# Kernel tuning notes

Measured on AMD Instinct MI355X. Metric: run time of the kernel, lower is better.

Reference implementation:

```python
import jax, jax.numpy as jnp
import numpy as np

EMBED_DIM = 1024
NUM_HEADS = 16
HEAD_DIM = EMBED_DIM // NUM_HEADS


def setup_inputs() -> dict:
    key = jax.random.key(0)
    ks = jax.random.split(key, 11)
    B, S, E = 4, 2048, EMBED_DIM
    s = 1.0 / np.sqrt(E)
    return {
        "q": jax.random.normal(ks[0], (B, S, E), jnp.float32),
        "k": jax.random.normal(ks[1], (B, S, E), jnp.float32),
        "v": jax.random.normal(ks[2], (B, S, E), jnp.float32),
        "Wq": jax.random.uniform(ks[3], (E, E), jnp.float32, -s, s),
        "bq": jax.random.uniform(ks[4], (E,), jnp.float32, -s, s),
        "Wk": jax.random.uniform(ks[5], (E, E), jnp.float32, -s, s),
        "bk": jax.random.uniform(ks[6], (E,), jnp.float32, -s, s),
        "Wv": jax.random.uniform(ks[7], (E, E), jnp.float32, -s, s),
        "bv": jax.random.uniform(ks[8], (E,), jnp.float32, -s, s),
        "Wo": jax.random.uniform(ks[9], (E, E), jnp.float32, -s, s),
        "bo": jax.random.uniform(ks[10], (E,), jnp.float32, -s, s),
    }


def _split_heads(x):
    B, S, E = x.shape
    return x.reshape(B, S, NUM_HEADS, HEAD_DIM).transpose(0, 2, 1, 3)  # [B,H,S,D]


def reference(q, k, v, Wq, bq, Wk, bk, Wv, bv, Wo, bo):
    # torch Linear: x @ W.T + b
    Q = _split_heads(q @ Wq.T + bq)
    K = _split_heads(k @ Wk.T + bk)
    V = _split_heads(v @ Wv.T + bv)
    scale = 1.0 / jnp.sqrt(jnp.float32(HEAD_DIM))
    scores = jnp.einsum("bhqd,bhkd->bhqk", Q, K) * scale  # [B,H,S,S]
    weights = jax.nn.softmax(scores, axis=-1)
    ctx = jnp.einsum("bhqk,bhkd->bhqd", weights, V)
    B, H, S, D = ctx.shape
    merged = ctx.transpose(0, 2, 1, 3).reshape(B, S, H * D)
    out = merged @ Wo.T + bo
    return out, weights
```

## Files before the change

kernel.cpp:

```cpp
#include <hip/hip_runtime.h>
#include <hip/hip_bf16.h>

typedef __bf16 bf16x8 __attribute__((ext_vector_type(8)));
typedef __bf16 bf16x4 __attribute__((ext_vector_type(4)));
typedef float f32x4 __attribute__((ext_vector_type(4)));

constexpr size_t XQ_OFF = 0;
constexpr size_t WQ_OFF = 25165824;
constexpr size_t Q_OFF  = 29360128;
constexpr size_t KK_OFF = 37748736;
constexpr size_t VT_OFF = 46137344;
constexpr size_t CTX_OFF= 54525952;

__device__ __forceinline__ void gload16(const void* g, void* s) {
    __builtin_amdgcn_global_load_lds((__attribute__((address_space(1))) void*)g,
                                     (__attribute__((address_space(3))) void*)s, 16, 0, 0);
}
#define WAIT_VM0()   asm volatile("s_waitcnt vmcnt(0)" ::: "memory")
#define WAIT_VM4()   asm volatile("s_waitcnt vmcnt(4)" ::: "memory")
#define WAIT_VM8()   asm volatile("s_waitcnt vmcnt(8)" ::: "memory")
#define WAIT_LGKM0() asm volatile("s_waitcnt lgkmcnt(0)" ::: "memory")
#define BAR()        __builtin_amdgcn_s_barrier()

__global__ __launch_bounds__(256) void convert_k(
    const float* __restrict__ q, const float* __restrict__ k, const float* __restrict__ v,
    const float* __restrict__ Wq, const float* __restrict__ Wk, const float* __restrict__ Wv,
    const float* __restrict__ Wo, __bf16* __restrict__ ws) {
    int id = blockIdx.x * 256 + threadIdx.x;
    const int NX = 1048576;
    const int NW = 131072;
    const float* src; size_t dst; int local;
    if (id < 3 * NX) {
        int z = id / NX; local = id - z * NX;
        src = (z == 0) ? q : ((z == 1) ? k : v);
        dst = XQ_OFF + (size_t)z * 8388608;
    } else {
        int i2 = id - 3 * NX;
        int z = i2 / NW; local = i2 - z * NW;
        src = (z == 0) ? Wq : ((z == 1) ? Wk : ((z == 2) ? Wv : Wo));
        dst = WQ_OFF + (size_t)z * 1048576;
    }
    const float4* s4 = (const float4*)(src + (size_t)local * 8);
    float4 a = s4[0], b = s4[1];
    bf16x8 o;
    o[0]=(__bf16)a.x; o[1]=(__bf16)a.y; o[2]=(__bf16)a.z; o[3]=(__bf16)a.w;
    o[4]=(__bf16)b.x; o[5]=(__bf16)b.y; o[6]=(__bf16)b.z; o[7]=(__bf16)b.w;
    *(bf16x8*)(ws + dst + (size_t)local * 8) = o;
}

template<int MODE>
__global__ __launch_bounds__(256) void gemm_k(
    __bf16* __restrict__ ws,
    const float* __restrict__ bq, const float* __restrict__ bk,
    const float* __restrict__ bv, const float* __restrict__ bo,
    float* __restrict__ out) {
    const int K = 1024;
    unsigned n = blockIdx.x + 64u * (blockIdx.y + 8u * blockIdx.z);
    unsigned cpx = (MODE == 0) ? 192u : 64u;
    unsigned m_ = (n & 7u) * cpx + (n >> 3);
    unsigned bx = m_ & 63u;
    unsigned rest = m_ >> 6;
    unsigned by = rest & 7u;
    unsigned bz = rest >> 3;

    int z = (int)bz;
    const __bf16* A; const __bf16* Bm; const float* bias;
    if (MODE == 0) {
        A    = ws + XQ_OFF + (size_t)z * 8388608;
        Bm   = ws + WQ_OFF + (size_t)z * 1048576;
        bias = (z == 0) ? bq : ((z == 1) ? bk : bv);
    } else {
        A    = ws + CTX_OFF;
        Bm   = ws + WQ_OFF + (size_t)3 * 1048576;
        bias = bo;
    }
    int row0 = (int)bx * 128, col0 = (int)by * 128;
    __shared__ __align__(16) __bf16 As[2][128 * 32];
    __shared__ __align__(16) __bf16 Bs[2][128 * 32];
    int t = threadIdx.x, lane = t & 63, w = t >> 6;
    int wr = w >> 1, wc = w & 1;
    f32x4 acc[4][4];
#pragma unroll
    for (int i = 0; i < 4; ++i)
#pragma unroll
        for (int j = 0; j < 4; ++j) acc[i][j] = (f32x4){0.f, 0.f, 0.f, 0.f};

    auto stage = [&](int buf, int kt) {
#pragma unroll
        for (int i = 0; i < 2; ++i) {
            int e = ((i * 4 + w) * 64 + lane) * 8;
            int r = e >> 5, c = e & 31;
            gload16(A  + (size_t)(row0 + r) * K + kt + c, &As[buf][e]);
            gload16(Bm + (size_t)(col0 + r) * K + kt + c, &Bs[buf][e]);
        }
    };

    stage(0, 0);
    int cur = 0;
    for (int kt = 0; kt < K; kt += 32) {
        bool nx = kt + 32 < K;
        if (nx) { stage(cur ^ 1, kt + 32); WAIT_VM4(); }
        else    { WAIT_VM0(); }
        BAR();
        const __bf16* Ac = As[cur];
        const __bf16* Bc = Bs[cur];
        bf16x8 af[4], bfr[4];
#pragma unroll
        for (int f = 0; f < 4; ++f) {
            af[f]  = *(const bf16x8*)&Ac[(wr * 64 + f * 16 + (lane & 15)) * 32 + (lane >> 4) * 8];
            bfr[f] = *(const bf16x8*)&Bc[(wc * 64 + f * 16 + (lane & 15)) * 32 + (lane >> 4) * 8];
        }
#pragma unroll
        for (int fr = 0; fr < 4; ++fr)
#pragma unroll
            for (int fc = 0; fc < 4; ++fc)
                acc[fr][fc] = __builtin_amdgcn_mfma_f32_16x16x32_bf16(af[fr], bfr[fc], acc[fr][fc], 0, 0, 0);
        WAIT_LGKM0();
        BAR();
        cur ^= 1;
    }

    if (MODE == 0) {
        __bf16* dqk = ws + Q_OFF + (size_t)z * 8388608;
        __bf16* dvt = ws + VT_OFF;
#pragma unroll
        for (int fr = 0; fr < 4; ++fr)
#pragma unroll
            for (int fc = 0; fc < 4; ++fc)
#pragma unroll
                for (int r = 0; r < 4; ++r) {
                    int m = row0 + wr * 64 + fr * 16 + ((lane >> 4) << 2) + r;
                    int nn = col0 + wc * 64 + fc * 16 + (lane & 15);
                    float val = acc[fr][fc][r] + bias[nn];
                    int bb = m >> 11, s = m & 2047, h = nn >> 6, d = nn & 63;
                    size_t bh = (size_t)bb * 16 + h;
                    if (z < 2) dqk[bh * 131072 + (size_t)s * 64 + d] = (__bf16)val;
                    else       dvt[bh * 131072 + (size_t)d * 2048 + s] = (__bf16)val;
                }
    } else {
#pragma unroll
        for (int fr = 0; fr < 4; ++fr)
#pragma unroll
            for (int fc = 0; fc < 4; ++fc)
#pragma unroll
                for (int r = 0; r < 4; ++r) {
                    int m = row0 + wr * 64 + fr * 16 + ((lane >> 4) << 2) + r;
                    int nn = col0 + wc * 64 + fc * 16 + (lane & 15);
                    out[(size_t)m * 1024 + nn] = acc[fr][fc][r] + bias[nn];
                }
    }
}

__global__ __launch_bounds__(512) void rowsum_k(const __bf16* __restrict__ ws,
                                                float* __restrict__ rs_out) {
    unsigned n = blockIdx.x + 8u * blockIdx.y;
    unsigned m = (n & 7u) * 64u + (n >> 3);
    int bh = (int)(m >> 3);
    int q0 = (int)(m & 7u) * 256;
    const __bf16* Qb = ws + Q_OFF  + (size_t)bh * 131072;
    const __bf16* Kb = ws + KK_OFF + (size_t)bh * 131072;
    __shared__ __align__(16) __bf16 Ks[2][64 * 64];
    int t = threadIdx.x, lane = t & 63, w = t >> 6, g = lane >> 4;
    const float SCALE = 0.125f;

    bf16x8 aq[2][2];
#pragma unroll
    for (int f = 0; f < 2; ++f) {
        int qr = q0 + w * 32 + f * 16 + (lane & 15);
        aq[f][0] = *(const bf16x8*)&Qb[(size_t)qr * 64 + g * 8];
        aq[f][1] = *(const bf16x8*)&Qb[(size_t)qr * 64 + 32 + g * 8];
    }

    { int r = t >> 3, c8 = t & 7;
      gload16(Kb + (size_t)r * 64 + ((c8 ^ (r & 7)) << 3), &Ks[0][t * 8]); }
    WAIT_VM0(); BAR();

    float rs[8] = {0.f,0.f,0.f,0.f,0.f,0.f,0.f,0.f};
    int cur = 0;
    for (int kt = 0; kt < 2048; kt += 64) {
        bool nx = kt < 1984;
        if (nx) {
            int r = t >> 3, c8 = t & 7;
            gload16(Kb + (size_t)(kt + 64 + r) * 64 + ((c8 ^ (r & 7)) << 3), &Ks[cur ^ 1][t * 8]);
        }
        const __bf16* Kc = Ks[cur];
        __builtin_amdgcn_s_setprio(1);
#pragma unroll
        for (int kc = 0; kc < 4; ++kc) {
            int krow = kc * 16 + (lane & 15);
            bf16x8 b0 = *(const bf16x8*)((const char*)Kc + krow * 128 + ((g * 16) ^ ((krow & 7) << 4)));
            bf16x8 b1 = *(const bf16x8*)((const char*)Kc + krow * 128 + (((4 + g) * 16) ^ ((krow & 7) << 4)));
#pragma unroll
            for (int f = 0; f < 2; ++f) {
                f32x4 s = (f32x4){0.f, 0.f, 0.f, 0.f};
                s = __builtin_amdgcn_mfma_f32_16x16x32_bf16(aq[f][0], b0, s, 0, 0, 0);
                s = __builtin_amdgcn_mfma_f32_16x16x32_bf16(aq[f][1], b1, s, 0, 0, 0);
#pragma unroll
                for (int r4 = 0; r4 < 4; ++r4) rs[f * 4 + r4] += __expf(s[r4] * SCALE);
            }
        }
        __builtin_amdgcn_s_setprio(0);
        WAIT_LGKM0();
        if (nx) WAIT_VM0();
        BAR();
        cur ^= 1;
    }
#pragma unroll
    for (int msk = 1; msk < 16; msk <<= 1)
#pragma unroll
        for (int i = 0; i < 8; ++i) rs[i] += __shfl_xor(rs[i], msk);
    if ((lane & 15) == 0) {
#pragma unroll
        for (int f = 0; f < 2; ++f)
#pragma unroll
            for (int r4 = 0; r4 < 4; ++r4)
                rs_out[(size_t)bh * 2048 + q0 + w * 32 + f * 16 + g * 4 + r4] = rs[f * 4 + r4];
    }
}

__global__ __launch_bounds__(512) void attnw_k(const __bf16* __restrict__ ws,
                                               const float* __restrict__ rsf,
                                               __bf16* __restrict__ wsw,
                                               float* __restrict__ wout) {
    unsigned n = blockIdx.x + 8u * blockIdx.y;
    unsigned m = (n & 7u) * 64u + (n >> 3);
    int bh = (int)(m >> 3);
    int q0 = (int)(m & 7u) * 256;

    const __bf16* Qb = ws + Q_OFF  + (size_t)bh * 131072;
    const __bf16* Kb = ws + KK_OFF + (size_t)bh * 131072;
    const __bf16* Vb = ws + VT_OFF + (size_t)bh * 131072;
    __bf16* ctx = wsw + CTX_OFF;

    int t = threadIdx.x, lane = t & 63, w = t >> 6, g = lane >> 4, q = lane & 15;
    __shared__ __align__(16) __bf16 Ks[2][64 * 64];
    __shared__ __align__(16) __bf16 Vts[2][64 * 64];
    __shared__ __align__(16) __bf16 Pf[256 * 64];
    const float SCALE = 0.125f;

    bf16x8 aq[2][2];
#pragma unroll
    for (int f = 0; f < 2; ++f) {
        int qr = q0 + w * 32 + f * 16 + q;
        aq[f][0] = *(const bf16x8*)&Qb[(size_t)qr * 64 + g * 8];
        aq[f][1] = *(const bf16x8*)&Qb[(size_t)qr * 64 + 32 + g * 8];
    }
    float rinv[2];
#pragma unroll
    for (int f = 0; f < 2; ++f)
        rinv[f] = 1.f / rsf[(size_t)bh * 2048 + q0 + w * 32 + f * 16 + q];

    { int r = t >> 3, c8 = t & 7;
      gload16(Kb + (size_t)r * 64   + ((c8 ^ (r & 7)) << 3), &Ks[0][t * 8]);
      gload16(Vb + (size_t)r * 2048 + ((c8 ^ (r & 7)) << 3), &Vts[0][t * 8]); }
    WAIT_VM0(); BAR();

    f32x4 cacc[2][4];
#pragma unroll
    for (int f = 0; f < 2; ++f)
#pragma unroll
        for (int dc = 0; dc < 4; ++dc) cacc[f][dc] = (f32x4){0.f, 0.f, 0.f, 0.f};

    int cur = 0;
    for (int kt = 0; kt < 2048; kt += 64) {
        bool nx = kt < 1984;
        if (nx) {
            int r = t >> 3, c8 = t & 7;
            gload16(Kb + (size_t)(kt + 64 + r) * 64 + ((c8 ^ (r & 7)) << 3), &Ks[cur ^ 1][t * 8]);
            gload16(Vb + (size_t)r * 2048 + (kt + 64) + ((c8 ^ (r & 7)) << 3), &Vts[cur ^ 1][t * 8]);
        }
        const __bf16* Kc = Ks[cur];
        const __bf16* Vc = Vts[cur];

        int2 pk[2][4];
        __builtin_amdgcn_s_setprio(1);
#pragma unroll
        for (int kc = 0; kc < 4; ++kc) {
            int krow = kc * 16 + q;
            bf16x8 b0 = *(const bf16x8*)((const char*)Kc + krow * 128 + ((g * 16) ^ ((krow & 7) << 4)));
            bf16x8 b1 = *(const bf16x8*)((const char*)Kc + krow * 128 + (((4 + g) * 16) ^ ((krow & 7) << 4)));
#pragma unroll
            for (int f = 0; f < 2; ++f) {
                f32x4 s = (f32x4){0.f, 0.f, 0.f, 0.f};
                s = __builtin_amdgcn_mfma_f32_16x16x32_bf16(b0, aq[f][0], s, 0, 0, 0);
                s = __builtin_amdgcn_mfma_f32_16x16x32_bf16(b1, aq[f][1], s, 0, 0, 0);
                bf16x4 p4;
#pragma unroll
                for (int r4 = 0; r4 < 4; ++r4)
                    p4[r4] = (__bf16)(__expf(s[r4] * SCALE) * rinv[f]);
                int2 pki = __builtin_bit_cast(int2, p4);
                pk[f][kc] = pki;
                int row_l = w * 32 + f * 16 + q;
                int cw = (kc * 4 + g) ^ (row_l & 7);
                *(int2*)((char*)Pf + row_l * 128 + cw * 8) = pki;
            }
        }
        __builtin_amdgcn_s_setprio(0);
        WAIT_LGKM0();
        __builtin_amdgcn_sched_barrier(0);
        BAR();

#pragma unroll
        for (int i = 0; i < 8; ++i) {
            int idx = t + 512 * i;
            int r = idx >> 4, u = idx & 15;
            int cu_ = u ^ (r & 7);
            int2 d = *(const int2*)((const char*)Pf + r * 128 + cu_ * 8);
            f32x4 v;
            v[0] = __builtin_bit_cast(float, d.x << 16);
            v[1] = __builtin_bit_cast(float, d.x & (int)0xffff0000);
            v[2] = __builtin_bit_cast(float, d.y << 16);
            v[3] = __builtin_bit_cast(float, d.y & (int)0xffff0000);
            float* dst = wout + ((size_t)bh * 2048 + q0 + r) * 2048 + kt + u * 4;
            *(f32x4*)dst = v;
        }

        int src0 = q + ((lane & 16) << 1);
        int src1 = src0 + 16;
        bool hi = lane >= 32;
        __builtin_amdgcn_s_setprio(1);
#pragma unroll
        for (int f = 0; f < 2; ++f) {
#pragma unroll
            for (int ks = 0; ks < 2; ++ks) {
                int2 A0 = pk[f][2 * ks], A1 = pk[f][2 * ks + 1];
                int l0a = __shfl(A0.x, src0), l0b = __shfl(A1.x, src0);
                int l1a = __shfl(A0.y, src0), l1b = __shfl(A1.y, src0);
                int h0a = __shfl(A0.x, src1), h0b = __shfl(A1.x, src1);
                int h1a = __shfl(A0.y, src1), h1b = __shfl(A1.y, src1);
                int4 ai;
                ai.x = hi ? l0b : l0a;
                ai.y = hi ? l1b : l1a;
                ai.z = hi ? h0b : h0a;
                ai.w = hi ? h1b : h1a;
                bf16x8 ap = __builtin_bit_cast(bf16x8, ai);
#pragma unroll
                for (int dc = 0; dc < 4; ++dc) {
                    int vrow = dc * 16 + q;
                    bf16x8 bv = *(const bf16x8*)((const char*)Vc + vrow * 128 + ((ks * 64 + g * 16) ^ ((vrow & 7) << 4)));
                    cacc[f][dc] = __builtin_amdgcn_mfma_f32_16x16x32_bf16(ap, bv, cacc[f][dc], 0, 0, 0);
                }
            }
        }
        __builtin_amdgcn_s_setprio(0);
        WAIT_LGKM0();
        if (nx) { WAIT_VM8(); BAR(); }
        cur ^= 1;
    }

    int bb = bh >> 4, h = bh & 15;
#pragma unroll
    for (int f = 0; f < 2; ++f)
#pragma unroll
        for (int dc = 0; dc < 4; ++dc)
#pragma unroll
            for (int r4 = 0; r4 < 4; ++r4) {
                int qg = q0 + w * 32 + f * 16 + (g << 2) + r4;
                int d = dc * 16 + q;
                ctx[((size_t)bb * 2048 + qg) * 1024 + h * 64 + d] = (__bf16)cacc[f][dc][r4];
            }
}

extern "C" void kernel_launch(void* const* d_in, const int* in_sizes, int n_in,
                              void* d_out, int out_size, void* d_ws, size_t ws_size,
                              hipStream_t stream) {
    const float* q  = (const float*)d_in[0];
    const float* k  = (const float*)d_in[1];
    const float* v  = (const float*)d_in[2];
    const float* Wq = (const float*)d_in[3];
    const float* bq = (const float*)d_in[4];
    const float* Wk = (const float*)d_in[5];
    const float* bk = (const float*)d_in[6];
    const float* Wv = (const float*)d_in[7];
    const float* bv = (const float*)d_in[8];
    const float* Wo = (const float*)d_in[9];
    const float* bo = (const float*)d_in[10];
    __bf16* ws = (__bf16*)d_ws;
    float* out  = (float*)d_out;
    float* wout = out + 8388608;
    float* rsum = (float*)d_ws;

    convert_k<<<dim3(14336), dim3(256), 0, stream>>>(q, k, v, Wq, Wk, Wv, Wo, ws);
    gemm_k<0><<<dim3(64, 8, 3), dim3(256), 0, stream>>>(ws, bq, bk, bv, bo, out);
    rowsum_k<<<dim3(8, 64), dim3(512), 0, stream>>>(ws, rsum);
    attnw_k<<<dim3(8, 64), dim3(512), 0, stream>>>(ws, rsum, ws, wout);
    gemm_k<1><<<dim3(64, 8, 1), dim3(256), 0, stream>>>(ws, bq, bk, bv, bo, out);
}
```

Before: 518.7 us.

## Halve attnw query tile and write weights via register shuffles instead of LDS

```diff
diff --git a/kernel.cpp b/kernel.cpp
--- a/kernel.cpp
+++ b/kernel.cpp
@@ -18,7 +18,6 @@
 }
 #define WAIT_VM0()   asm volatile("s_waitcnt vmcnt(0)" ::: "memory")
 #define WAIT_VM4()   asm volatile("s_waitcnt vmcnt(4)" ::: "memory")
-#define WAIT_VM8()   asm volatile("s_waitcnt vmcnt(8)" ::: "memory")
 #define WAIT_LGKM0() asm volatile("s_waitcnt lgkmcnt(0)" ::: "memory")
 #define BAR()        __builtin_amdgcn_s_barrier()
 
@@ -222,10 +221,10 @@
                                                const float* __restrict__ rsf,
                                                __bf16* __restrict__ wsw,
                                                float* __restrict__ wout) {
-    unsigned n = blockIdx.x + 8u * blockIdx.y;
-    unsigned m = (n & 7u) * 64u + (n >> 3);
-    int bh = (int)(m >> 3);
-    int q0 = (int)(m & 7u) * 256;
+    unsigned n = blockIdx.x + 16u * blockIdx.y;
+    unsigned m = (n & 7u) * 128u + (n >> 3);
+    int bh = (int)(m >> 4);
+    int q0 = (int)(m & 15u) * 128;
 
     const __bf16* Qb = ws + Q_OFF  + (size_t)bh * 131072;
     const __bf16* Kb = ws + KK_OFF + (size_t)bh * 131072;
@@ -235,31 +234,24 @@
     int t = threadIdx.x, lane = t & 63, w = t >> 6, g = lane >> 4, q = lane & 15;
     __shared__ __align__(16) __bf16 Ks[2][64 * 64];
     __shared__ __align__(16) __bf16 Vts[2][64 * 64];
-    __shared__ __align__(16) __bf16 Pf[256 * 64];
     const float SCALE = 0.125f;
 
-    bf16x8 aq[2][2];
-#pragma unroll
-    for (int f = 0; f < 2; ++f) {
-        int qr = q0 + w * 32 + f * 16 + q;
-        aq[f][0] = *(const bf16x8*)&Qb[(size_t)qr * 64 + g * 8];
-        aq[f][1] = *(const bf16x8*)&Qb[(size_t)qr * 64 + 32 + g * 8];
-    }
-    float rinv[2];
-#pragma unroll
-    for (int f = 0; f < 2; ++f)
-        rinv[f] = 1.f / rsf[(size_t)bh * 2048 + q0 + w * 32 + f * 16 + q];
+    bf16x8 aq0, aq1;
+    {
+        int qr = q0 + w * 16 + q;
+        aq0 = *(const bf16x8*)&Qb[(size_t)qr * 64 + g * 8];
+        aq1 = *(const bf16x8*)&Qb[(size_t)qr * 64 + 32 + g * 8];
+    }
+    float rinv = 1.f / rsf[(size_t)bh * 2048 + q0 + w * 16 + q];
 
     { int r = t >> 3, c8 = t & 7;
       gload16(Kb + (size_t)r * 64   + ((c8 ^ (r & 7)) << 3), &Ks[0][t * 8]);
       gload16(Vb + (size_t)r * 2048 + ((c8 ^ (r & 7)) << 3), &Vts[0][t * 8]); }
     WAIT_VM0(); BAR();
 
-    f32x4 cacc[2][4];
-#pragma unroll
-    for (int f = 0; f < 2; ++f)
-#pragma unroll
-        for (int dc = 0; dc < 4; ++dc) cacc[f][dc] = (f32x4){0.f, 0.f, 0.f, 0.f};
+    f32x4 cacc[4];
+#pragma unroll
+    for (int dc = 0; dc < 4; ++dc) cacc[dc] = (f32x4){0.f, 0.f, 0.f, 0.f};
 
     int cur = 0;
     for (int kt = 0; kt < 2048; kt += 64) {
@@ -272,46 +264,43 @@
         const __bf16* Kc = Ks[cur];
         const __bf16* Vc = Vts[cur];
 
-        int2 pk[2][4];
+        int2 pk[4];
         __builtin_amdgcn_s_setprio(1);
 #pragma unroll
         for (int kc = 0; kc < 4; ++kc) {
             int krow = kc * 16 + q;
             bf16x8 b0 = *(const bf16x8*)((const char*)Kc + krow * 128 + ((g * 16) ^ ((krow & 7) << 4)));
             bf16x8 b1 = *(const bf16x8*)((const char*)Kc + krow * 128 + (((4 + g) * 16) ^ ((krow & 7) << 4)));
-#pragma unroll
-            for (int f = 0; f < 2; ++f) {
-                f32x4 s = (f32x4){0.f, 0.f, 0.f, 0.f};
-                s = __builtin_amdgcn_mfma_f32_16x16x32_bf16(b0, aq[f][0], s, 0, 0, 0);
-                s = __builtin_amdgcn_mfma_f32_16x16x32_bf16(b1, aq[f][1], s, 0, 0, 0);
-                bf16x4 p4;
-#pragma unroll
-                for (int r4 = 0; r4 < 4; ++r4)
-                    p4[r4] = (__bf16)(__expf(s[r4] * SCALE) * rinv[f]);
-                int2 pki = __builtin_bit_cast(int2, p4);
-                pk[f][kc] = pki;
-                int row_l = w * 32 + f * 16 + q;
-                int cw = (kc * 4 + g) ^ (row_l & 7);
-                *(int2*)((char*)Pf + row_l * 128 + cw * 8) = pki;
-            }
+            f32x4 s = (f32x4){0.f, 0.f, 0.f, 0.f};
+            s = __builtin_amdgcn_mfma_f32_16x16x32_bf16(b0, aq0, s, 0, 0, 0);
+            s = __builtin_amdgcn_mfma_f32_16x16x32_bf16(b1, aq1, s, 0, 0, 0);
+            bf16x4 p4;
+#pragma unroll
+            for (int r4 = 0; r4 < 4; ++r4)
+                p4[r4] = (__bf16)(__expf(s[r4] * SCALE) * rinv);
+            pk[kc] = __builtin_bit_cast(int2, p4);
         }
         __builtin_amdgcn_s_setprio(0);
-        WAIT_LGKM0();
-        __builtin_amdgcn_sched_barrier(0);
-        BAR();
-
-#pragma unroll
-        for (int i = 0; i < 8; ++i) {
-            int idx = t + 512 * i;
-            int r = idx >> 4, u = idx & 15;
-            int cu_ = u ^ (r & 7);
-            int2 d = *(const int2*)((const char*)Pf + r * 128 + cu_ * 8);
+
+        int c16 = lane & 15;
+        int sel = c16 >> 2;
+        int pbase = (c16 & 3) << 4;
+#pragma unroll
+        for (int j = 0; j < 4; ++j) {
+            int r = (lane >> 4) + 4 * j;
+            int p = pbase | r;
+            int sx0 = __shfl(pk[0].x, p), sy0 = __shfl(pk[0].y, p);
+            int sx1 = __shfl(pk[1].x, p), sy1 = __shfl(pk[1].y, p);
+            int sx2 = __shfl(pk[2].x, p), sy2 = __shfl(pk[2].y, p);
+            int sx3 = __shfl(pk[3].x, p), sy3 = __shfl(pk[3].y, p);
+            int vx = sel == 0 ? sx0 : (sel == 1 ? sx1 : (sel == 2 ? sx2 : sx3));
+            int vy = sel == 0 ? sy0 : (sel == 1 ? sy1 : (sel == 2 ? sy2 : sy3));
             f32x4 v;
-            v[0] = __builtin_bit_cast(float, d.x << 16);
-            v[1] = __builtin_bit_cast(float, d.x & (int)0xffff0000);
-            v[2] = __builtin_bit_cast(float, d.y << 16);
-            v[3] = __builtin_bit_cast(float, d.y & (int)0xffff0000);
-            float* dst = wout + ((size_t)bh * 2048 + q0 + r) * 2048 + kt + u * 4;
+            v[0] = __builtin_bit_cast(float, vx << 16);
+            v[1] = __builtin_bit_cast(float, vx & (int)0xffff0000);
+            v[2] = __builtin_bit_cast(float, vy << 16);
+            v[3] = __builtin_bit_cast(float, vy & (int)0xffff0000);
+            float* dst = wout + ((size_t)bh * 2048 + q0 + w * 16 + r) * 2048 + kt + c16 * 4;
             *(f32x4*)dst = v;
         }
 
@@ -320,45 +309,40 @@
         bool hi = lane >= 32;
         __builtin_amdgcn_s_setprio(1);
 #pragma unroll
-        for (int f = 0; f < 2; ++f) {
-#pragma unroll
-            for (int ks = 0; ks < 2; ++ks) {
-                int2 A0 = pk[f][2 * ks], A1 = pk[f][2 * ks + 1];
-                int l0a = __shfl(A0.x, src0), l0b = __shfl(A1.x, src0);
-                int l1a = __shfl(A0.y, src0), l1b = __shfl(A1.y, src0);
-                int h0a = __shfl(A0.x, src1), h0b = __shfl(A1.x, src1);
-                int h1a = __shfl(A0.y, src1), h1b = __shfl(A1.y, src1);
-                int4 ai;
-                ai.x = hi ? l0b : l0a;
-                ai.y = hi ? l1b : l1a;
-                ai.z = hi ? h0b : h0a;
-                ai.w = hi ? h1b : h1a;
-                bf16x8 ap = __builtin_bit_cast(bf16x8, ai);
-#pragma unroll
-                for (int dc = 0; dc < 4; ++dc) {
-                    int vrow = dc * 16 + q;
-                    bf16x8 bv = *(const bf16x8*)((const char*)Vc + vrow * 128 + ((ks * 64 + g * 16) ^ ((vrow & 7) << 4)));
-                    cacc[f][dc] = __builtin_amdgcn_mfma_f32_16x16x32_bf16(ap, bv, cacc[f][dc], 0, 0, 0);
-                }
+        for (int ks = 0; ks < 2; ++ks) {
+            int2 A0 = pk[2 * ks], A1 = pk[2 * ks + 1];
+            int l0a = __shfl(A0.x, src0), l0b = __shfl(A1.x, src0);
+            int l1a = __shfl(A0.y, src0), l1b = __shfl(A1.y, src0);
+            int h0a = __shfl(A0.x, src1), h0b = __shfl(A1.x, src1);
+            int h1a = __shfl(A0.y, src1), h1b = __shfl(A1.y, src1);
+            int4 ai;
+            ai.x = hi ? l0b : l0a;
+            ai.y = hi ? l1b : l1a;
+            ai.z = hi ? h0b : h0a;
+            ai.w = hi ? h1b : h1a;
+            bf16x8 ap = __builtin_bit_cast(bf16x8, ai);
+#pragma unroll
+            for (int dc = 0; dc < 4; ++dc) {
+                int vrow = dc * 16 + q;
+                bf16x8 bv = *(const bf16x8*)((const char*)Vc + vrow * 128 + ((ks * 64 + g * 16) ^ ((vrow & 7) << 4)));
+                cacc[dc] = __builtin_amdgcn_mfma_f32_16x16x32_bf16(ap, bv, cacc[dc], 0, 0, 0);
             }
         }
         __builtin_amdgcn_s_setprio(0);
         WAIT_LGKM0();
-        if (nx) { WAIT_VM8(); BAR(); }
+        if (nx) { WAIT_VM4(); BAR(); }
         cur ^= 1;
     }
 
     int bb = bh >> 4, h = bh & 15;
 #pragma unroll
-    for (int f = 0; f < 2; ++f)
-#pragma unroll
-        for (int dc = 0; dc < 4; ++dc)
-#pragma unroll
-            for (int r4 = 0; r4 < 4; ++r4) {
-                int qg = q0 + w * 32 + f * 16 + (g << 2) + r4;
-                int d = dc * 16 + q;
-                ctx[((size_t)bb * 2048 + qg) * 1024 + h * 64 + d] = (__bf16)cacc[f][dc][r4];
-            }
+    for (int dc = 0; dc < 4; ++dc)
+#pragma unroll
+        for (int r4 = 0; r4 < 4; ++r4) {
+            int qg = q0 + w * 16 + (g << 2) + r4;
+            int d = dc * 16 + q;
+            ctx[((size_t)bb * 2048 + qg) * 1024 + h * 64 + d] = (__bf16)cacc[dc][r4];
+        }
 }
 
 extern "C" void kernel_launch(void* const* d_in, const int* in_sizes, int n_in,
@@ -383,6 +367,6 @@
     convert_k<<<dim3(14336), dim3(256), 0, stream>>>(q, k, v, Wq, Wk, Wv, Wo, ws);
     gemm_k<0><<<dim3(64, 8, 3), dim3(256), 0, stream>>>(ws, bq, bk, bv, bo, out);
     rowsum_k<<<dim3(8, 64), dim3(512), 0, stream>>>(ws, rsum);
-    attnw_k<<<dim3(8, 64), dim3(512), 0, stream>>>(ws, rsum, ws, wout);
+    attnw_k<<<dim3(16, 64), dim3(512), 0, stream>>>(ws, rsum, ws, wout);
     gemm_k<1><<<dim3(64, 8, 1), dim3(256), 0, stream>>>(ws, bq, bk, bv, bo, out);
 }
```

Measured after the change: 524.1 us. Within noise of the previous version (+1.0%).
